# Optimization experiments

Hardware: AMD Instinct MI355X
Metric: run time of the kernel (lower is better)

## Reference

```python
import jax, jax.numpy as jnp
import numpy as np

T, B, I, H = 512, 256, 256, 256


def setup_inputs() -> dict:
    key = jax.random.key(0)
    ks = jax.random.split(key, 7)
    sk = 1.0 / np.sqrt(H)
    u = lambda k, shape: jax.random.uniform(k, shape, jnp.float32, -sk, sk)
    return {
        "x": jax.random.normal(ks[0], (T, B, I), jnp.float32),
        "W_ih": u(ks[1], (3 * H, I)),   # rows ordered [r, z, n] as in torch GRUCell
        "W_hh": u(ks[2], (3 * H, H)),
        "b_ih": u(ks[3], (3 * H,)),
        "b_hh": u(ks[4], (3 * H,)),
        "W_out": u(ks[5], (1, H)),
        "b_out": u(ks[6], (1,)),
    }


def _gru_forward(x, W_ih, W_hh, b_ih, b_hh):
    # Precompute input projections for all timesteps in one big GEMM: [T,B,3H]
    gi_all = jnp.einsum("tbi,gi->tbg", x, W_ih) + b_ih

    def step(h, gi):
        gh = h @ W_hh.T + b_hh                      # [B, 3H]
        i_r, i_z, i_n = jnp.split(gi, 3, axis=-1)
        h_r, h_z, h_n = jnp.split(gh, 3, axis=-1)
        r = jax.nn.sigmoid(i_r + h_r)
        z = jax.nn.sigmoid(i_z + h_z)
        n = jnp.tanh(i_n + r * h_n)
        h_new = (1.0 - z) * n + z * h
        return h_new, None

    h0 = jnp.zeros((x.shape[1], W_hh.shape[1]), x.dtype)
    h_final, _ = jax.lax.scan(step, h0, gi_all)
    return h_final


def reference(x, W_ih, W_hh, b_ih, b_hh, W_out, b_out):
    h = _gru_forward(x, W_ih, W_hh, b_ih, b_hh)
    return jax.nn.sigmoid(h @ W_out.T + b_out)      # [B, 1]
```

## Files before the change

### kernel.cpp

```cpp
#include <hip/hip_runtime.h>
#include <hip/hip_bf16.h>


#define TT 512
#define BB 256
#define II 256
#define HH 256

#define SRZ (-1.4426950408889634f)
#define SN  (2.8853900817779268f)

typedef __attribute__((ext_vector_type(8))) short short8;
typedef __attribute__((ext_vector_type(4))) float f32x4;

__device__ __forceinline__ unsigned short rne_bf16(float f) {
  union { float f; unsigned u; } v; v.f = f;
  unsigned r = v.u + 0x7FFFu + ((v.u >> 16) & 1u);
  return (unsigned short)(r >> 16);
}
__device__ __forceinline__ float bf2f(unsigned short b) {
  union { unsigned u; float f; } v; v.u = ((unsigned)b) << 16;
  return v.f;
}
__device__ __forceinline__ float sigm(float x) { return 1.0f / (1.0f + __expf(-x)); }
__device__ __forceinline__ float tanhfast(float x) {
  return 1.0f - 2.0f / (__expf(2.0f * x) + 1.0f);
}

__device__ __forceinline__ short8 ldw8(const float* __restrict__ p) {
  float4 a = *reinterpret_cast<const float4*>(p);
  float4 b = *reinterpret_cast<const float4*>(p + 4);
  short8 r;
  r[0] = (short)rne_bf16(a.x); r[1] = (short)rne_bf16(a.y);
  r[2] = (short)rne_bf16(a.z); r[3] = (short)rne_bf16(a.w);
  r[4] = (short)rne_bf16(b.x); r[5] = (short)rne_bf16(b.y);
  r[6] = (short)rne_bf16(b.z); r[7] = (short)rne_bf16(b.w);
  return r;
}
__device__ __forceinline__ short8 ldw8s(const float* __restrict__ p, float s) {
  float4 a = *reinterpret_cast<const float4*>(p);
  float4 b = *reinterpret_cast<const float4*>(p + 4);
  short8 r;
  r[0] = (short)rne_bf16(a.x * s); r[1] = (short)rne_bf16(a.y * s);
  r[2] = (short)rne_bf16(a.z * s); r[3] = (short)rne_bf16(a.w * s);
  r[4] = (short)rne_bf16(b.x * s); r[5] = (short)rne_bf16(b.y * s);
  r[6] = (short)rne_bf16(b.z * s); r[7] = (short)rne_bf16(b.w * s);
  return r;
}

#define SWZ(m, k) ((m) * 256 + ((k) ^ ((m) * 16)))

__device__ __forceinline__ void stage16(unsigned short* lds,
                                        const float* __restrict__ src, int tid) {
  int m = tid >> 6, k0 = (tid & 63) << 2;
  float4 v = *reinterpret_cast<const float4*>(src + m * 256 + k0);
  ushort4 b;
  b.x = rne_bf16(v.x); b.y = rne_bf16(v.y);
  b.z = rne_bf16(v.z); b.w = rne_bf16(v.w);
  *reinterpret_cast<ushort4*>(lds + SWZ(m, k0)) = b;
}

__device__ __forceinline__ short8 lda(const unsigned short* lds, int lane, int c) {
  int m = lane & 15;
  int k0 = c * 32 + (lane >> 4) * 8;
  return *reinterpret_cast<const short8*>(lds + SWZ(m, k0));
}

__device__ __forceinline__ f32x4 mfma16(short8 a, short8 b, f32x4 c) {
  return __builtin_amdgcn_mfma_f32_16x16x32_bf16(a, b, c, 0, 0, 0);
}

__global__ __launch_bounds__(1024)
__attribute__((amdgpu_waves_per_eu(4, 4)))
void gi_gemm2(const float* __restrict__ x, const float* __restrict__ Wih,
              const float* __restrict__ bih, const float* __restrict__ bhh,
              unsigned short* __restrict__ gi, int ntiles) {
  __shared__ unsigned short ax[2][4096];
  int tid = threadIdx.x, l = tid & 63, wg = tid >> 6;
  int g4 = l >> 4, i15 = l & 15;
  int g = blockIdx.x % 3;
  int tgrp = blockIdx.x / 3;
  int ngrp = gridDim.x / 3;
  int nb = 16 * wg + i15;
  float scale = (g == 2) ? SN : SRZ;
  float bias = (g == 2) ? bih[512 + nb] : (bih[g * 256 + nb] + bhh[g * 256 + nb]);
  short8 wf[8];
#pragma unroll
  for (int c = 0; c < 8; ++c)
    wf[c] = ldw8(Wih + (size_t)(g * 256 + nb) * 256 + c * 32 + g4 * 8);

  int tile = tgrp;
  if (tile >= ntiles) return;
  stage16(ax[0], x + (size_t)tile * 4096, tid);
  __syncthreads();
  int cur = 0;
  int slot = (nb >> 5) * 512 + (((g4 << 4) | i15)) * 8 + ((nb >> 4) & 1) * 4;
  while (true) {
    int nxt_tile = tile + ngrp;
    if (nxt_tile < ntiles) stage16(ax[cur ^ 1], x + (size_t)nxt_tile * 4096, tid);
    short8 a[8];
#pragma unroll
    for (int c = 0; c < 8; ++c) a[c] = lda(ax[cur], l, c);
    f32x4 acc = {0, 0, 0, 0};
#pragma unroll
    for (int c = 0; c < 8; ++c) acc = mfma16(a[c], wf[c], acc);
    ushort4 o;
    o.x = rne_bf16((acc[0] + bias) * scale);
    o.y = rne_bf16((acc[1] + bias) * scale);
    o.z = rne_bf16((acc[2] + bias) * scale);
    o.w = rne_bf16((acc[3] + bias) * scale);
    *reinterpret_cast<ushort4*>(&gi[(size_t)tile * 12288 + g * 4096 + slot]) = o;
    if (nxt_tile >= ntiles) break;
    __syncthreads();
    cur ^= 1;
    tile = nxt_tile;
  }
}

__global__ __launch_bounds__(512)
__attribute__((amdgpu_waves_per_eu(2, 2)))
void gru_step2(const float* __restrict__ Whh, const float* __restrict__ bhh,
               const float* __restrict__ Wout, const float* __restrict__ bout,
               const unsigned short* __restrict__ gi, float* __restrict__ hchk,
               float* __restrict__ out, int t0, int nt) {
  __shared__ __align__(16) unsigned char arena[147456];
  unsigned short* ldsn = (unsigned short*)arena;
  unsigned short* hbuf0 = (unsigned short*)(arena + 131072);
  unsigned short* hbuf1 = (unsigned short*)(arena + 139264);

  int tid = threadIdx.x, l = tid & 63, w = tid >> 6;
  int g4 = l >> 4, i15 = l & 15;
  int bx = blockIdx.x, b0 = bx * 16;

  short8 wr[2][8], wz[2][8];
  float cn[2];
#pragma unroll
  for (int tl = 0; tl < 2; ++tl) {
    int j = 32 * w + 16 * tl + i15;
#pragma unroll
    for (int c = 0; c < 8; ++c) {
      int ko = c * 32 + g4 * 8;
      wr[tl][c] = ldw8s(Whh + (size_t)j * 256 + ko, SRZ);
      wz[tl][c] = ldw8s(Whh + (size_t)(256 + j) * 256 + ko, SRZ);
      short8 fn = ldw8s(Whh + (size_t)(512 + j) * 256 + ko, SN);
      *reinterpret_cast<short8*>(&ldsn[(size_t)(((w * 2 + tl) * 8 + c) * 64 + l) * 8]) = fn;
    }
    cn[tl] = SN * bhh[512 + j];
  }

  f32x4 h[2] = {{0, 0, 0, 0}, {0, 0, 0, 0}};
  if (t0 == 0) {
    for (int idx = tid; idx < 4096; idx += 512) hbuf0[idx] = 0;
  } else {
#pragma unroll
    for (int tl = 0; tl < 2; ++tl) {
      int j = 32 * w + 16 * tl + i15;
#pragma unroll
      for (int q = 0; q < 4; ++q) {
        float hv = hchk[(size_t)(b0 + 4 * g4 + q) * 256 + j];
        h[tl][q] = hv;
        hbuf0[SWZ(4 * g4 + q, j)] = rne_bf16(hv);
      }
    }
  }
  __syncthreads();

  int lslot = w * 512 + l * 8;
  short8 gc[3], gn_[3];
  {
    const unsigned short* p = gi + (size_t)bx * 12288 + lslot;
    gc[0] = *reinterpret_cast<const short8*>(p);
    gc[1] = *reinterpret_cast<const short8*>(p + 4096);
    gc[2] = *reinterpret_cast<const short8*>(p + 8192);
  }

  const unsigned short* nbase = ldsn + (size_t)l * 8 + (size_t)(w * 2) * 8 * 64 * 8;

  for (int lt = 0; lt < nt; ++lt) {
    if (lt + 1 < nt) {
      const unsigned short* p = gi + ((size_t)(lt + 1) * 16 + bx) * 12288 + lslot;
      gn_[0] = *reinterpret_cast<const short8*>(p);
      gn_[1] = *reinterpret_cast<const short8*>(p + 4096);
      gn_[2] = *reinterpret_cast<const short8*>(p + 8192);
    }
    const unsigned short* hb = (lt & 1) ? hbuf1 : hbuf0;
    unsigned short* hw = (lt & 1) ? hbuf0 : hbuf1;

    f32x4 ar[2] = {{0, 0, 0, 0}, {0, 0, 0, 0}};
    f32x4 az[2] = {{0, 0, 0, 0}, {0, 0, 0, 0}};
    f32x4 an[2] = {{0, 0, 0, 0}, {0, 0, 0, 0}};
#pragma unroll
    for (int half = 0; half < 2; ++half) {
      short8 ah[4];
#pragma unroll
      for (int cc = 0; cc < 4; ++cc) ah[cc] = lda(hb, l, half * 4 + cc);
#pragma unroll
      for (int cc = 0; cc < 4; ++cc) {
        int c = half * 4 + cc;
#pragma unroll
        for (int tl = 0; tl < 2; ++tl) {
          short8 fn = *reinterpret_cast<const short8*>(nbase + (tl * 8 + c) * 512);
          ar[tl] = mfma16(ah[cc], wr[tl][c], ar[tl]);
          az[tl] = mfma16(ah[cc], wz[tl][c], az[tl]);
          an[tl] = mfma16(ah[cc], fn, an[tl]);
        }
      }
    }
#pragma unroll
    for (int tl = 0; tl < 2; ++tl) {
#pragma unroll
      for (int q = 0; q < 4; ++q) {
        float gr = bf2f((unsigned short)gc[0][tl * 4 + q]);
        float gz = bf2f((unsigned short)gc[1][tl * 4 + q]);
        float gv = bf2f((unsigned short)gc[2][tl * 4 + q]);
        float r = __builtin_amdgcn_rcpf(1.0f + __builtin_amdgcn_exp2f(ar[tl][q] + gr));
        float zz = __builtin_amdgcn_rcpf(1.0f + __builtin_amdgcn_exp2f(az[tl][q] + gz));
        float y = gv + r * (an[tl][q] + cn[tl]);
        float nn = 1.0f - 2.0f * __builtin_amdgcn_rcpf(1.0f + __builtin_amdgcn_exp2f(y));
        float hq = nn + zz * (h[tl][q] - nn);
        h[tl][q] = hq;
        hw[SWZ(4 * g4 + q, 32 * w + 16 * tl + i15)] = rne_bf16(hq);
      }
    }
    gc[0] = gn_[0]; gc[1] = gn_[1]; gc[2] = gn_[2];
    __syncthreads();
  }

  if (t0 + nt < TT) {
#pragma unroll
    for (int tl = 0; tl < 2; ++tl) {
      int j = 32 * w + 16 * tl + i15;
#pragma unroll
      for (int q = 0; q < 4; ++q)
        hchk[(size_t)(b0 + 4 * g4 + q) * 256 + j] = h[tl][q];
    }
  } else {
    float* hfin = (float*)arena;
#pragma unroll
    for (int tl = 0; tl < 2; ++tl) {
      int j = 32 * w + 16 * tl + i15;
#pragma unroll
      for (int q = 0; q < 4; ++q) hfin[(4 * g4 + q) * 256 + j] = h[tl][q];
    }
    __syncthreads();
#pragma unroll
    for (int rr = 0; rr < 2; ++rr) {
      int r = 2 * w + rr;
      float s = 0.0f;
#pragma unroll
      for (int i = 0; i < 4; ++i) {
        int k = l + 64 * i;
        s += hfin[r * 256 + k] * Wout[k];
      }
#pragma unroll
      for (int off = 32; off > 0; off >>= 1) s += __shfl_xor(s, off, 64);
      if (l == 0) out[b0 + r] = sigm(s + bout[0]);
    }
  }
}

__global__ __launch_bounds__(1024, 1) void gru_fused_legacy(
    const float* __restrict__ x, const float* __restrict__ Wih,
    const float* __restrict__ Whh, const float* __restrict__ bih,
    const float* __restrict__ bhh, const float* __restrict__ Wout,
    const float* __restrict__ bout, float* __restrict__ out) {
  __shared__ unsigned short hbuf[2][16 * 256];
  __shared__ unsigned short xbuf[2][16 * 256];
  __shared__ float hfin[16][256];
  int tid = threadIdx.x, lane = tid & 63, w = tid >> 6;
  int i15 = lane & 15, g4 = lane >> 4;
  int b0 = blockIdx.x * 16;
  int j = 16 * w + i15;

  short8 whh0[8], whh1[8], whh2[8], wih0[8], wih1[8], wih2[8];
#pragma unroll
  for (int c = 0; c < 8; ++c) {
    int ko = c * 32 + g4 * 8;
    whh0[c] = ldw8(Whh + (size_t)j * 256 + ko);
    whh1[c] = ldw8(Whh + (size_t)(256 + j) * 256 + ko);
    whh2[c] = ldw8(Whh + (size_t)(512 + j) * 256 + ko);
    wih0[c] = ldw8(Wih + (size_t)j * 256 + ko);
    wih1[c] = ldw8(Wih + (size_t)(256 + j) * 256 + ko);
    wih2[c] = ldw8(Wih + (size_t)(512 + j) * 256 + ko);
  }
  float bias_r = bih[j] + bhh[j];
  float bias_z = bih[256 + j] + bhh[256 + j];
  float bihn = bih[512 + j], bhhn = bhh[512 + j];

  f32x4 h = {0, 0, 0, 0};
  for (int idx = tid; idx < 16 * 256; idx += 1024) hbuf[0][idx] = 0;
  stage16(xbuf[0], x + (size_t)b0 * II, tid);
  __syncthreads();

  for (int lt = 0; lt < TT; ++lt) {
    int cur = lt & 1, nxt = cur ^ 1;
    short8 ah[8], axf[8];
#pragma unroll
    for (int c = 0; c < 8; ++c) ah[c] = lda(hbuf[cur], lane, c);
#pragma unroll
    for (int c = 0; c < 8; ++c) axf[c] = lda(xbuf[cur], lane, c);
    f32x4 gr = {0, 0, 0, 0}, gz = {0, 0, 0, 0}, gn = {0, 0, 0, 0};
    f32x4 ar = {0, 0, 0, 0}, az = {0, 0, 0, 0}, an = {0, 0, 0, 0};
#pragma unroll
    for (int c = 0; c < 8; ++c) {
      gr = mfma16(axf[c], wih0[c], gr);
      gz = mfma16(axf[c], wih1[c], gz);
      gn = mfma16(axf[c], wih2[c], gn);
    }
    if (lt + 1 < TT)
      stage16(xbuf[nxt], x + ((size_t)(lt + 1) * BB + b0) * II, tid);
#pragma unroll
    for (int c = 0; c < 8; ++c) {
      ar = mfma16(ah[c], whh0[c], ar);
      az = mfma16(ah[c], whh1[c], az);
      an = mfma16(ah[c], whh2[c], an);
    }
#pragma unroll
    for (int q = 0; q < 4; ++q) {
      float r = sigm(ar[q] + gr[q] + bias_r);
      float zz = sigm(az[q] + gz[q] + bias_z);
      float nn = tanhfast(gn[q] + bihn + r * (an[q] + bhhn));
      float hq = (1.0f - zz) * nn + zz * h[q];
      h[q] = hq;
      hbuf[nxt][SWZ(g4 * 4 + q, j)] = rne_bf16(hq);
    }
    __syncthreads();
  }
#pragma unroll
  for (int q = 0; q < 4; ++q) hfin[g4 * 4 + q][j] = h[q];
  __syncthreads();
  float s = 0.0f;
#pragma unroll
  for (int i = 0; i < 4; ++i) {
    int k = lane + 64 * i;
    s += hfin[w][k] * Wout[k];
  }
#pragma unroll
  for (int off = 32; off > 0; off >>= 1) s += __shfl_xor(s, off, 64);
  if (lane == 0) out[b0 + w] = sigm(s + bout[0]);
}

extern "C" void kernel_launch(void* const* d_in, const int* in_sizes, int n_in,
                              void* d_out, int out_size, void* d_ws, size_t ws_size,
                              hipStream_t stream) {
  const float* x    = (const float*)d_in[0];
  const float* Wih  = (const float*)d_in[1];
  const float* Whh  = (const float*)d_in[2];
  const float* bih  = (const float*)d_in[3];
  const float* bhh  = (const float*)d_in[4];
  const float* Wout = (const float*)d_in[5];
  const float* bout = (const float*)d_in[6];
  float* out = (float*)d_out;

  const size_t HBYTES = (size_t)BB * HH * sizeof(float);
  const size_t STEP_BYTES = (size_t)16 * 12288 * sizeof(unsigned short);
  size_t gi_cap = ws_size > HBYTES ? ws_size - HBYTES : 0;
  long tc = (long)(gi_cap / STEP_BYTES);
  if (tc > TT) tc = TT;

  if (tc >= 32) {
    float* hchk = (float*)d_ws;
    unsigned short* gi = (unsigned short*)((char*)d_ws + HBYTES);
    for (int t0 = 0; t0 < TT; t0 += (int)tc) {
      int nt = (TT - t0) < (int)tc ? (TT - t0) : (int)tc;
      gi_gemm2<<<dim3(3 * 1024), dim3(1024), 0, stream>>>(
          x + (size_t)t0 * BB * II, Wih, bih, bhh, gi, nt * 16);
      gru_step2<<<dim3(16), dim3(512), 0, stream>>>(
          Whh, bhh, Wout, bout, gi, hchk, out, t0, nt);
    }
  } else {
    gru_fused_legacy<<<dim3(16), dim3(1024), 0, stream>>>(
        x, Wih, Whh, bih, bhh, Wout, bout, out);
  }
}
```

Before: 1.078 ms.

## Restructure gi GEMM and stream gate inputs into LDS via async loads

The input-projection GEMM is rewritten so each block computes all three gates for 4 tiles per iteration. The x staging is double-buffered across tiles, and a packed per-lane output layout is written. The recurrent step kernel keeps all three W_hh gate fragments in registers instead of reading the n-gate weights from LDS. It prefetches the next timestep's gate inputs with global_load_lds into a double-buffered LDS buffer, replacing the register prefetch. This removes per-step LDS weight reads and shortens the serial step's critical path, at the cost of higher register pressure and a reliance on async LDS load ordering being correct under the existing barrier.

Result: slower. 1.463 ms (+35.7%).

```diff
diff --git a/kernel.cpp b/kernel.cpp
--- a/kernel.cpp
+++ b/kernel.cpp
@@ -50,16 +50,6 @@
 
 #define SWZ(m, k) ((m) * 256 + ((k) ^ ((m) * 16)))
 
-__device__ __forceinline__ void stage16(unsigned short* lds,
-                                        const float* __restrict__ src, int tid) {
-  int m = tid >> 6, k0 = (tid & 63) << 2;
-  float4 v = *reinterpret_cast<const float4*>(src + m * 256 + k0);
-  ushort4 b;
-  b.x = rne_bf16(v.x); b.y = rne_bf16(v.y);
-  b.z = rne_bf16(v.z); b.w = rne_bf16(v.w);
-  *reinterpret_cast<ushort4*>(lds + SWZ(m, k0)) = b;
-}
-
 __device__ __forceinline__ short8 lda(const unsigned short* lds, int lane, int c) {
   int m = lane & 15;
   int k0 = c * 32 + (lane >> 4) * 8;
@@ -70,69 +60,110 @@
   return __builtin_amdgcn_mfma_f32_16x16x32_bf16(a, b, c, 0, 0, 0);
 }
 
-__global__ __launch_bounds__(1024)
-__attribute__((amdgpu_waves_per_eu(4, 4)))
-void gi_gemm2(const float* __restrict__ x, const float* __restrict__ Wih,
+__device__ __forceinline__ void gload_lds16(const void* g, void* lds) {
+  __builtin_amdgcn_global_load_lds(
+      (const __attribute__((address_space(1))) unsigned int*)g,
+      (__attribute__((address_space(3))) unsigned int*)lds, 16, 0, 0);
+}
+
+__global__ __launch_bounds__(512, 2)
+void gi_gemm4(const float* __restrict__ x, const float* __restrict__ Wih,
               const float* __restrict__ bih, const float* __restrict__ bhh,
               unsigned short* __restrict__ gi, int ntiles) {
-  __shared__ unsigned short ax[2][4096];
-  int tid = threadIdx.x, l = tid & 63, wg = tid >> 6;
-  int g4 = l >> 4, i15 = l & 15;
-  int g = blockIdx.x % 3;
-  int tgrp = blockIdx.x / 3;
-  int ngrp = gridDim.x / 3;
-  int nb = 16 * wg + i15;
-  float scale = (g == 2) ? SN : SRZ;
-  float bias = (g == 2) ? bih[512 + nb] : (bih[g * 256 + nb] + bhh[g * 256 + nb]);
-  short8 wf[8];
-#pragma unroll
-  for (int c = 0; c < 8; ++c)
-    wf[c] = ldw8(Wih + (size_t)(g * 256 + nb) * 256 + c * 32 + g4 * 8);
-
-  int tile = tgrp;
-  if (tile >= ntiles) return;
-  stage16(ax[0], x + (size_t)tile * 4096, tid);
-  __syncthreads();
-  int cur = 0;
-  int slot = (nb >> 5) * 512 + (((g4 << 4) | i15)) * 8 + ((nb >> 4) & 1) * 4;
-  while (true) {
-    int nxt_tile = tile + ngrp;
-    if (nxt_tile < ntiles) stage16(ax[cur ^ 1], x + (size_t)nxt_tile * 4096, tid);
-    short8 a[8];
-#pragma unroll
-    for (int c = 0; c < 8; ++c) a[c] = lda(ax[cur], l, c);
-    f32x4 acc = {0, 0, 0, 0};
-#pragma unroll
-    for (int c = 0; c < 8; ++c) acc = mfma16(a[c], wf[c], acc);
-    ushort4 o;
-    o.x = rne_bf16((acc[0] + bias) * scale);
-    o.y = rne_bf16((acc[1] + bias) * scale);
-    o.z = rne_bf16((acc[2] + bias) * scale);
-    o.w = rne_bf16((acc[3] + bias) * scale);
-    *reinterpret_cast<ushort4*>(&gi[(size_t)tile * 12288 + g * 4096 + slot]) = o;
-    if (nxt_tile >= ntiles) break;
+  __shared__ unsigned short ax[2][4][4096];
+  const int tid = threadIdx.x, l = tid & 63, w = tid >> 6;
+  const int g4 = l >> 4, i15 = l & 15;
+
+  short8 wf[3][2][8];
+  float bs[3][2];
+#pragma unroll
+  for (int tl = 0; tl < 2; ++tl) {
+    int j = 32 * w + 16 * tl + i15;
+#pragma unroll
+    for (int c = 0; c < 8; ++c) {
+      int ko = c * 32 + g4 * 8;
+      wf[0][tl][c] = ldw8s(Wih + (size_t)j * 256 + ko, SRZ);
+      wf[1][tl][c] = ldw8s(Wih + (size_t)(256 + j) * 256 + ko, SRZ);
+      wf[2][tl][c] = ldw8s(Wih + (size_t)(512 + j) * 256 + ko, SN);
+    }
+    bs[0][tl] = SRZ * (bih[j] + bhh[j]);
+    bs[1][tl] = SRZ * (bih[256 + j] + bhh[256 + j]);
+    bs[2][tl] = SN * bih[512 + j];
+  }
+
+  int tpb = ((ntiles + 255) >> 8);
+  tpb = (tpb + 3) & ~3;
+  const int tstart = blockIdx.x * tpb;
+  if (tstart >= ntiles) return;
+  const int niter = tpb >> 2;
+
+  auto stage4 = [&](int buf, int t0) {
+#pragma unroll
+    for (int p = 0; p < 8; ++p) {
+      int f = p * 512 + tid;
+      int tb = f >> 10, r4 = f & 1023;
+      int m = r4 >> 6, k0 = (r4 & 63) << 2;
+      int tsrc = t0 + tb; if (tsrc >= ntiles) tsrc = ntiles - 1;
+      float4 v = *reinterpret_cast<const float4*>(x + (size_t)tsrc * 4096 + m * 256 + k0);
+      ushort4 b;
+      b.x = rne_bf16(v.x); b.y = rne_bf16(v.y);
+      b.z = rne_bf16(v.z); b.w = rne_bf16(v.w);
+      *reinterpret_cast<ushort4*>(&ax[buf][tb][SWZ(m, k0)]) = b;
+    }
+  };
+
+  stage4(0, tstart);
+  for (int it = 0; it < niter; ++it) {
     __syncthreads();
-    cur ^= 1;
-    tile = nxt_tile;
-  }
-}
-
-__global__ __launch_bounds__(512)
-__attribute__((amdgpu_waves_per_eu(2, 2)))
-void gru_step2(const float* __restrict__ Whh, const float* __restrict__ bhh,
+    if (it + 1 < niter) stage4((it + 1) & 1, tstart + (it + 1) * 4);
+    const int cur = it & 1;
+#pragma unroll
+    for (int tb = 0; tb < 4; ++tb) {
+      int tile = tstart + it * 4 + tb;
+      if (tile >= ntiles) break;
+      f32x4 acc[3][2];
+#pragma unroll
+      for (int g = 0; g < 3; ++g)
+#pragma unroll
+        for (int tl = 0; tl < 2; ++tl) acc[g][tl] = (f32x4){0, 0, 0, 0};
+#pragma unroll
+      for (int c = 0; c < 8; ++c) {
+        short8 ah = lda(ax[cur][tb], l, c);
+#pragma unroll
+        for (int g = 0; g < 3; ++g) {
+          acc[g][0] = mfma16(ah, wf[g][0][c], acc[g][0]);
+          acc[g][1] = mfma16(ah, wf[g][1][c], acc[g][1]);
+        }
+      }
+      unsigned short* gp = gi + (size_t)tile * 12288 + w * 1536 + l * 24;
+#pragma unroll
+      for (int g = 0; g < 3; ++g) {
+        short8 o;
+#pragma unroll
+        for (int tl = 0; tl < 2; ++tl) {
+#pragma unroll
+          for (int q = 0; q < 4; ++q)
+            o[tl * 4 + q] = (short)rne_bf16(acc[g][tl][q] + bs[g][tl]);
+        }
+        *reinterpret_cast<short8*>(gp + g * 8) = o;
+      }
+    }
+  }
+}
+
+__global__ __launch_bounds__(512, 2)
+void gru_step3(const float* __restrict__ Whh, const float* __restrict__ bhh,
                const float* __restrict__ Wout, const float* __restrict__ bout,
                const unsigned short* __restrict__ gi, float* __restrict__ hchk,
                float* __restrict__ out, int t0, int nt) {
-  __shared__ __align__(16) unsigned char arena[147456];
-  unsigned short* ldsn = (unsigned short*)arena;
-  unsigned short* hbuf0 = (unsigned short*)(arena + 131072);
-  unsigned short* hbuf1 = (unsigned short*)(arena + 139264);
-
-  int tid = threadIdx.x, l = tid & 63, w = tid >> 6;
-  int g4 = l >> 4, i15 = l & 15;
-  int bx = blockIdx.x, b0 = bx * 16;
-
-  short8 wr[2][8], wz[2][8];
+  __shared__ unsigned short hbuf[2][4096];
+  __shared__ unsigned short gibuf[2][12288];
+  __shared__ float hfin[4096];
+  const int tid = threadIdx.x, l = tid & 63, w = tid >> 6;
+  const int g4 = l >> 4, i15 = l & 15;
+  const int bx = blockIdx.x, b0 = bx * 16;
+
+  short8 wf[3][2][8];
   float cn[2];
 #pragma unroll
   for (int tl = 0; tl < 2; ++tl) {
@@ -140,17 +171,16 @@
 #pragma unroll
     for (int c = 0; c < 8; ++c) {
       int ko = c * 32 + g4 * 8;
-      wr[tl][c] = ldw8s(Whh + (size_t)j * 256 + ko, SRZ);
-      wz[tl][c] = ldw8s(Whh + (size_t)(256 + j) * 256 + ko, SRZ);
-      short8 fn = ldw8s(Whh + (size_t)(512 + j) * 256 + ko, SN);
-      *reinterpret_cast<short8*>(&ldsn[(size_t)(((w * 2 + tl) * 8 + c) * 64 + l) * 8]) = fn;
+      wf[0][tl][c] = ldw8s(Whh + (size_t)j * 256 + ko, SRZ);
+      wf[1][tl][c] = ldw8s(Whh + (size_t)(256 + j) * 256 + ko, SRZ);
+      wf[2][tl][c] = ldw8s(Whh + (size_t)(512 + j) * 256 + ko, SN);
     }
     cn[tl] = SN * bhh[512 + j];
   }
 
   f32x4 h[2] = {{0, 0, 0, 0}, {0, 0, 0, 0}};
   if (t0 == 0) {
-    for (int idx = tid; idx < 4096; idx += 512) hbuf0[idx] = 0;
+    for (int i = tid; i < 4096; i += 512) hbuf[0][i] = 0;
   } else {
 #pragma unroll
     for (int tl = 0; tl < 2; ++tl) {
@@ -159,70 +189,62 @@
       for (int q = 0; q < 4; ++q) {
         float hv = hchk[(size_t)(b0 + 4 * g4 + q) * 256 + j];
         h[tl][q] = hv;
-        hbuf0[SWZ(4 * g4 + q, j)] = rne_bf16(hv);
+        hbuf[0][SWZ(4 * g4 + q, j)] = rne_bf16(hv);
       }
     }
   }
+
+  const char* gsrc = (const char*)gi + (size_t)bx * 24576 + w * 3072 + (size_t)l * 48;
+#pragma unroll
+  for (int k = 0; k < 3; ++k)
+    gload_lds16(gsrc + k * 16, &gibuf[0][w * 1536 + k * 512]);
   __syncthreads();
 
-  int lslot = w * 512 + l * 8;
-  short8 gc[3], gn_[3];
-  {
-    const unsigned short* p = gi + (size_t)bx * 12288 + lslot;
-    gc[0] = *reinterpret_cast<const short8*>(p);
-    gc[1] = *reinterpret_cast<const short8*>(p + 4096);
-    gc[2] = *reinterpret_cast<const short8*>(p + 8192);
-  }
-
-  const unsigned short* nbase = ldsn + (size_t)l * 8 + (size_t)(w * 2) * 8 * 64 * 8;
-
   for (int lt = 0; lt < nt; ++lt) {
-    if (lt + 1 < nt) {
-      const unsigned short* p = gi + ((size_t)(lt + 1) * 16 + bx) * 12288 + lslot;
-      gn_[0] = *reinterpret_cast<const short8*>(p);
-      gn_[1] = *reinterpret_cast<const short8*>(p + 4096);
-      gn_[2] = *reinterpret_cast<const short8*>(p + 8192);
-    }
-    const unsigned short* hb = (lt & 1) ? hbuf1 : hbuf0;
-    unsigned short* hw = (lt & 1) ? hbuf0 : hbuf1;
-
-    f32x4 ar[2] = {{0, 0, 0, 0}, {0, 0, 0, 0}};
-    f32x4 az[2] = {{0, 0, 0, 0}, {0, 0, 0, 0}};
-    f32x4 an[2] = {{0, 0, 0, 0}, {0, 0, 0, 0}};
-#pragma unroll
-    for (int half = 0; half < 2; ++half) {
-      short8 ah[4];
-#pragma unroll
-      for (int cc = 0; cc < 4; ++cc) ah[cc] = lda(hb, l, half * 4 + cc);
-#pragma unroll
-      for (int cc = 0; cc < 4; ++cc) {
-        int c = half * 4 + cc;
-#pragma unroll
-        for (int tl = 0; tl < 2; ++tl) {
-          short8 fn = *reinterpret_cast<const short8*>(nbase + (tl * 8 + c) * 512);
-          ar[tl] = mfma16(ah[cc], wr[tl][c], ar[tl]);
-          az[tl] = mfma16(ah[cc], wz[tl][c], az[tl]);
-          an[tl] = mfma16(ah[cc], fn, an[tl]);
-        }
-      }
-    }
+    const int cur = lt & 1, nxt = cur ^ 1;
+    if (lt + 1 < nt) gsrc += 393216;
+#pragma unroll
+    for (int k = 0; k < 3; ++k)
+      gload_lds16(gsrc + k * 16, &gibuf[nxt][w * 1536 + k * 512]);
+
+    f32x4 aR[2] = {{0, 0, 0, 0}, {0, 0, 0, 0}};
+    f32x4 aZ[2] = {{0, 0, 0, 0}, {0, 0, 0, 0}};
+    f32x4 aN[2] = {{0, 0, 0, 0}, {0, 0, 0, 0}};
+    const unsigned short* hb = hbuf[cur];
+#pragma unroll
+    for (int c = 0; c < 8; ++c) {
+      short8 ah = lda(hb, l, c);
+      aR[0] = mfma16(ah, wf[0][0][c], aR[0]);
+      aR[1] = mfma16(ah, wf[0][1][c], aR[1]);
+      aZ[0] = mfma16(ah, wf[1][0][c], aZ[0]);
+      aZ[1] = mfma16(ah, wf[1][1][c], aZ[1]);
+      aN[0] = mfma16(ah, wf[2][0][c], aN[0]);
+      aN[1] = mfma16(ah, wf[2][1][c], aN[1]);
+    }
+
+    const unsigned short* gb = &gibuf[cur][w * 1536 + l * 8];
+    short8 gR = *reinterpret_cast<const short8*>(gb);
+    short8 gZ = *reinterpret_cast<const short8*>(gb + 512);
+    short8 gN = *reinterpret_cast<const short8*>(gb + 1024);
+
+    unsigned short* hw = hbuf[nxt];
 #pragma unroll
     for (int tl = 0; tl < 2; ++tl) {
+      int jx = 32 * w + 16 * tl + i15;
 #pragma unroll
       for (int q = 0; q < 4; ++q) {
-        float gr = bf2f((unsigned short)gc[0][tl * 4 + q]);
-        float gz = bf2f((unsigned short)gc[1][tl * 4 + q]);
-        float gv = bf2f((unsigned short)gc[2][tl * 4 + q]);
-        float r = __builtin_amdgcn_rcpf(1.0f + __builtin_amdgcn_exp2f(ar[tl][q] + gr));
-        float zz = __builtin_amdgcn_rcpf(1.0f + __builtin_amdgcn_exp2f(az[tl][q] + gz));
-        float y = gv + r * (an[tl][q] + cn[tl]);
+        float gr = bf2f((unsigned short)gR[tl * 4 + q]);
+        float gz = bf2f((unsigned short)gZ[tl * 4 + q]);
+        float gv = bf2f((unsigned short)gN[tl * 4 + q]);
+        float r  = __builtin_amdgcn_rcpf(1.0f + __builtin_amdgcn_exp2f(aR[tl][q] + gr));
+        float zz = __builtin_amdgcn_rcpf(1.0f + __builtin_amdgcn_exp2f(aZ[tl][q] + gz));
+        float y  = gv + r * (aN[tl][q] + cn[tl]);
         float nn = 1.0f - 2.0f * __builtin_amdgcn_rcpf(1.0f + __builtin_amdgcn_exp2f(y));
         float hq = nn + zz * (h[tl][q] - nn);
         h[tl][q] = hq;
-        hw[SWZ(4 * g4 + q, 32 * w + 16 * tl + i15)] = rne_bf16(hq);
+        hw[SWZ(4 * g4 + q, jx)] = rne_bf16(hq);
       }
     }
-    gc[0] = gn_[0]; gc[1] = gn_[1]; gc[2] = gn_[2];
     __syncthreads();
   }
 
@@ -235,7 +257,6 @@
         hchk[(size_t)(b0 + 4 * g4 + q) * 256 + j] = h[tl][q];
     }
   } else {
-    float* hfin = (float*)arena;
 #pragma unroll
     for (int tl = 0; tl < 2; ++tl) {
       int j = 32 * w + 16 * tl + i15;
@@ -289,7 +310,14 @@
 
   f32x4 h = {0, 0, 0, 0};
   for (int idx = tid; idx < 16 * 256; idx += 1024) hbuf[0][idx] = 0;
-  stage16(xbuf[0], x + (size_t)b0 * II, tid);
+  {
+    int m = tid >> 6, k0 = (tid & 63) << 2;
+    float4 v = *reinterpret_cast<const float4*>(x + (size_t)b0 * II + m * 256 + k0);
+    ushort4 b;
+    b.x = rne_bf16(v.x); b.y = rne_bf16(v.y);
+    b.z = rne_bf16(v.z); b.w = rne_bf16(v.w);
+    *reinterpret_cast<ushort4*>(&xbuf[0][SWZ(m, k0)]) = b;
+  }
   __syncthreads();
 
   for (int lt = 0; lt < TT; ++lt) {
@@ -307,8 +335,15 @@
       gz = mfma16(axf[c], wih1[c], gz);
       gn = mfma16(axf[c], wih2[c], gn);
     }
-    if (lt + 1 < TT)
-      stage16(xbuf[nxt], x + ((size_t)(lt + 1) * BB + b0) * II, tid);
+    if (lt + 1 < TT) {
+      int m = tid >> 6, k0 = (tid & 63) << 2;
+      float4 v = *reinterpret_cast<const float4*>(
+          x + ((size_t)(lt + 1) * BB + b0) * II + m * 256 + k0);
+      ushort4 b;
+      b.x = rne_bf16(v.x); b.y = rne_bf16(v.y);
+      b.z = rne_bf16(v.z); b.w = rne_bf16(v.w);
+      *reinterpret_cast<ushort4*>(&xbuf[nxt][SWZ(m, k0)]) = b;
+    }
 #pragma unroll
     for (int c = 0; c < 8; ++c) {
       ar = mfma16(ah[c], whh0[c], ar);
@@ -363,9 +398,9 @@
     unsigned short* gi = (unsigned short*)((char*)d_ws + HBYTES);
     for (int t0 = 0; t0 < TT; t0 += (int)tc) {
       int nt = (TT - t0) < (int)tc ? (TT - t0) : (int)tc;
-      gi_gemm2<<<dim3(3 * 1024), dim3(1024), 0, stream>>>(
+      gi_gemm4<<<dim3(256), dim3(512), 0, stream>>>(
           x + (size_t)t0 * BB * II, Wih, bih, bhh, gi, nt * 16);
-      gru_step2<<<dim3(16), dim3(512), 0, stream>>>(
+      gru_step3<<<dim3(16), dim3(512), 0, stream>>>(
           Whh, bhh, Wout, bout, gi, hchk, out, t0, nt);
     }
   } else {
```
